# Kernel optimization log

Hardware: AMD Instinct MI355X
Metric: run time of the kernel (lower is better)

## Reference

```python
import jax, jax.numpy as jnp
import numpy as np

IN_FEATURES = 4096
OUT_FEATURES = 11008
QMIN, QMAX = -128, 127


def setup_inputs() -> dict:
    key = jax.random.key(0)
    k_in, k_w, k_s, k_z, k_b = jax.random.split(key, 5)
    inp = jax.random.normal(k_in, (4, 2048, IN_FEATURES), dtype=jnp.float32)
    # int8 quantized weight in [qmin, qmax]
    weight_quantized = jax.random.randint(
        k_w, (OUT_FEATURES, IN_FEATURES), QMIN, QMAX + 1, dtype=jnp.int32
    ).astype(jnp.int8)
    # per-output-row scale / zero point (shape [out, 1] as in the module)
    weight_scale = jax.random.uniform(k_s, (OUT_FEATURES, 1), dtype=jnp.float32,
                                      minval=0.005, maxval=0.02)
    weight_zero_point = jax.random.uniform(k_z, (OUT_FEATURES, 1), dtype=jnp.float32,
                                           minval=-4.0, maxval=4.0)
    bias = jax.random.normal(k_b, (OUT_FEATURES,), dtype=jnp.float32) * 0.01
    return {
        "input": inp,
        "weight_quantized": weight_quantized,
        "weight_scale": weight_scale,
        "weight_zero_point": weight_zero_point,
        "bias": bias,
    }


def reference(input, weight_quantized, weight_scale, weight_zero_point, bias):
    # Dequantize: per-row affine, W_f32[o, i] = (q[o, i] - zp[o]) * scale[o]
    weight_float = (weight_quantized.astype(jnp.float32) - weight_zero_point) * weight_scale
    # F.linear: y = x @ W^T + b   -> [B, S, out]
    out = jnp.einsum("bsi,oi->bso", input, weight_float) + bias
    return out
```

## Files before the change

kernel.cpp:

```cpp
#include <hip/hip_runtime.h>
#include <hip/hip_bf16.h>

#define K_DIM 4096
#define N_DIM 11008
#define M_DIM 8192

typedef _Float16 f16;
typedef f16 f16x4 __attribute__((ext_vector_type(4)));
typedef f16 f16x8 __attribute__((ext_vector_type(8)));
typedef float f32x4 __attribute__((ext_vector_type(4)));

typedef __attribute__((address_space(1))) unsigned int gu32;
typedef __attribute__((address_space(3))) unsigned int lu32;

__device__ __forceinline__ void g2l16(const void* gp, void* lp) {
    __builtin_amdgcn_global_load_lds((gu32*)gp, (lu32*)lp, 16, 0, 0);
}

__global__ __launch_bounds__(256) void convw_kernel(const int* __restrict__ Wq,
                                                    f16* __restrict__ Wh) {
    const size_t n4 = (size_t)N_DIM * K_DIM / 4;
    const size_t stride = (size_t)gridDim.x * 256;
    const int4* src = (const int4*)Wq;
    f16x4* dst = (f16x4*)Wh;
    for (size_t i = (size_t)blockIdx.x * 256 + threadIdx.x; i < n4; i += stride) {
        int4 a = src[i];
        f16x4 o = {(f16)a.x, (f16)a.y, (f16)a.z, (f16)a.w};
        dst[i] = o;
    }
}

__global__ __launch_bounds__(256) void convx_kernel(const float* __restrict__ X,
                                                    f16* __restrict__ Xh,
                                                    float* __restrict__ rs) {
    const int row = blockIdx.x;
    const int t = threadIdx.x;
    const float4* xr = (const float4*)(X + (size_t)row * K_DIM);
    f16x4* xo = (f16x4*)(Xh + (size_t)row * K_DIM);
    float s = 0.f;
#pragma unroll
    for (int j = 0; j < 4; ++j) {
        float4 v = xr[t + 256 * j];
        f16x4 h = {(f16)v.x, (f16)v.y, (f16)v.z, (f16)v.w};
        xo[t + 256 * j] = h;
        s += (float)h[0] + (float)h[1] + (float)h[2] + (float)h[3];
    }
#pragma unroll
    for (int off = 32; off > 0; off >>= 1) s += __shfl_down(s, off);
    __shared__ float part[4];
    if ((t & 63) == 0) part[t >> 6] = s;
    __syncthreads();
    if (t == 0) rs[row] = part[0] + part[1] + part[2] + part[3];
}

__global__ __launch_bounds__(256, 2)
void qlin_gemm(const f16* __restrict__ Xh, const f16* __restrict__ Wh,
               const float* __restrict__ scale, const float* __restrict__ zp,
               const float* __restrict__ bias, const float* __restrict__ rowsum,
               float* __restrict__ out) {
    __shared__ char lx[8192];
    __shared__ char lw[8192];

    const int tid = threadIdx.x;
    const int l = tid & 63;
    const int w = tid >> 6;
    const int wm = w & 1;
    const int wn = w >> 1;
    const int q = l >> 4;
    const int ln = l & 15;

    const int m0 = blockIdx.x * 128;
    const int n0 = blockIdx.y * 128;

    const int sg = (l & 3) ^ ((l >> 3) & 3);
    const size_t rowbytes = K_DIM * 2;

    const char* xg = (const char*)Xh + (size_t)(m0 + w * 16 + (l >> 2)) * rowbytes + sg * 16;
    const char* wg = (const char*)Wh + (size_t)(n0 + w * 16 + (l >> 2)) * rowbytes + sg * 16;
    char* lxp = lx + w * 1024 + l * 16;
    char* lwp = lw + w * 1024 + l * 16;

    const int rsw = (q ^ ((ln >> 1) & 3)) * 16;
    const char* lxr = lx + (wm * 64 + ln) * 64 + rsw;
    const char* lwr = lw + (wn * 64 + ln) * 64 + rsw;

    f32x4 acc[4][4] = {};

    for (int kt = 0; kt < 128; ++kt) {
        const size_t k0 = (size_t)kt * 64;
        g2l16(xg + k0, lxp);
        g2l16(xg + 64 * rowbytes + k0, lxp + 4096);
        g2l16(wg + k0, lwp);
        g2l16(wg + 64 * rowbytes + k0, lwp + 4096);
        __syncthreads();

        f16x8 af[4], bf[4];
#pragma unroll
        for (int i = 0; i < 4; ++i) af[i] = *(const f16x8*)(lxr + i * 1024);
#pragma unroll
        for (int j = 0; j < 4; ++j) bf[j] = *(const f16x8*)(lwr + j * 1024);
#pragma unroll
        for (int i = 0; i < 4; ++i)
#pragma unroll
            for (int j = 0; j < 4; ++j)
                acc[i][j] = __builtin_amdgcn_mfma_f32_16x16x32_f16(af[i], bf[j], acc[i][j], 0, 0, 0);
        __syncthreads();
    }

    float sc[4], zv[4], bv[4];
    int ncol[4];
#pragma unroll
    for (int j = 0; j < 4; ++j) {
        const int n = n0 + wn * 64 + j * 16 + ln;
        ncol[j] = n;
        sc[j] = scale[n];
        zv[j] = zp[n];
        bv[j] = bias[n];
    }
#pragma unroll
    for (int i = 0; i < 4; ++i) {
#pragma unroll
        for (int r = 0; r < 4; ++r) {
            const int m = m0 + wm * 64 + i * 16 + q * 4 + r;
            const float rsm = rowsum[m];
            const size_t rowoff = (size_t)m * N_DIM;
#pragma unroll
            for (int j = 0; j < 4; ++j) {
                out[rowoff + ncol[j]] = sc[j] * (acc[i][j][r] - zv[j] * rsm) + bv[j];
            }
        }
    }
}

extern "C" void kernel_launch(void* const* d_in, const int* in_sizes, int n_in,
                              void* d_out, int out_size, void* d_ws, size_t ws_size,
                              hipStream_t stream) {
    const float* X     = (const float*)d_in[0];
    const int*   Wq    = (const int*)d_in[1];
    const float* scale = (const float*)d_in[2];
    const float* zp    = (const float*)d_in[3];
    const float* bias  = (const float*)d_in[4];
    float* out = (float*)d_out;

    f16* Wh = (f16*)d_ws;
    f16* Xh = (f16*)((char*)d_ws + (size_t)N_DIM * K_DIM * 2);
    float* rowsum = (float*)((char*)d_ws + (size_t)N_DIM * K_DIM * 2 + (size_t)M_DIM * K_DIM * 2);

    convw_kernel<<<4096, 256, 0, stream>>>(Wq, Wh);
    convx_kernel<<<M_DIM, 256, 0, stream>>>(X, Xh, rowsum);

    dim3 grid(M_DIM / 128, N_DIM / 128);
    qlin_gemm<<<grid, 256, 0, stream>>>(Xh, Wh, scale, zp, bias, rowsum, out);
}
```

Before: 1.370 ms.

## Enlarge GEMM tile to 256x256 with double-buffered LDS and interleaved loads

```diff
diff --git a/kernel.cpp b/kernel.cpp
--- a/kernel.cpp
+++ b/kernel.cpp
@@ -1,9 +1,9 @@
 #include <hip/hip_runtime.h>
-#include <hip/hip_bf16.h>
 
 #define K_DIM 4096
 #define N_DIM 11008
 #define M_DIM 8192
+#define NT 64
 
 typedef _Float16 f16;
 typedef f16 f16x4 __attribute__((ext_vector_type(4)));
@@ -53,59 +53,128 @@
     if (t == 0) rs[row] = part[0] + part[1] + part[2] + part[3];
 }
 
-__global__ __launch_bounds__(256, 2)
+__global__ __launch_bounds__(512, 2)
 void qlin_gemm(const f16* __restrict__ Xh, const f16* __restrict__ Wh,
                const float* __restrict__ scale, const float* __restrict__ zp,
                const float* __restrict__ bias, const float* __restrict__ rowsum,
                float* __restrict__ out) {
-    __shared__ char lx[8192];
-    __shared__ char lw[8192];
-
-    const int tid = threadIdx.x;
-    const int l = tid & 63;
-    const int w = tid >> 6;
-    const int wm = w & 1;
-    const int wn = w >> 1;
+    extern __shared__ __align__(16) char smem[];
+
+    const int t = threadIdx.x;
+    const int l = t & 63;
+    const int w = t >> 6;
+    const int wm = w >> 2;
+    const int wn = w & 3;
     const int q = l >> 4;
     const int ln = l & 15;
 
-    const int m0 = blockIdx.x * 128;
-    const int n0 = blockIdx.y * 128;
-
-    const int sg = (l & 3) ^ ((l >> 3) & 3);
-    const size_t rowbytes = K_DIM * 2;
-
-    const char* xg = (const char*)Xh + (size_t)(m0 + w * 16 + (l >> 2)) * rowbytes + sg * 16;
-    const char* wg = (const char*)Wh + (size_t)(n0 + w * 16 + (l >> 2)) * rowbytes + sg * 16;
-    char* lxp = lx + w * 1024 + l * 16;
-    char* lwp = lw + w * 1024 + l * 16;
-
-    const int rsw = (q ^ ((ln >> 1) & 3)) * 16;
-    const char* lxr = lx + (wm * 64 + ln) * 64 + rsw;
-    const char* lwr = lw + (wn * 64 + ln) * 64 + rsw;
-
-    f32x4 acc[4][4] = {};
-
-    for (int kt = 0; kt < 128; ++kt) {
-        const size_t k0 = (size_t)kt * 64;
-        g2l16(xg + k0, lxp);
-        g2l16(xg + 64 * rowbytes + k0, lxp + 4096);
-        g2l16(wg + k0, lwp);
-        g2l16(wg + 64 * rowbytes + k0, lwp + 4096);
-        __syncthreads();
-
-        f16x8 af[4], bf[4];
-#pragma unroll
-        for (int i = 0; i < 4; ++i) af[i] = *(const f16x8*)(lxr + i * 1024);
-#pragma unroll
-        for (int j = 0; j < 4; ++j) bf[j] = *(const f16x8*)(lwr + j * 1024);
-#pragma unroll
-        for (int i = 0; i < 4; ++i)
-#pragma unroll
-            for (int j = 0; j < 4; ++j)
-                acc[i][j] = __builtin_amdgcn_mfma_f32_16x16x32_f16(af[i], bf[j], acc[i][j], 0, 0, 0);
-        __syncthreads();
-    }
+    const int m0 = blockIdx.x * 256;
+    const int n0 = blockIdx.y * 256;
+
+    const int srow = t >> 3;
+    const int sslot = (t & 7) ^ (srow & 7);
+    const char* xbase = (const char*)Xh + ((size_t)(m0 + srow) << 13) + (sslot << 4);
+    const char* wbase = (const char*)Wh + ((size_t)(n0 + srow) << 13) + (sslot << 4);
+    char* ldst = smem + t * 16;
+
+#define STG_A(p, c, T) g2l16(xbase + ((size_t)(c) << 19) + ((size_t)(T) << 7), ldst + (p)*65536 + (c)*8192)
+#define STG_B(p, c, T) g2l16(wbase + ((size_t)(c) << 19) + ((size_t)(T) << 7), ldst + (p)*65536 + 32768 + (c)*8192)
+#define SB __builtin_amdgcn_sched_barrier(0)
+#define BAR __builtin_amdgcn_s_barrier()
+#define LGKM0 asm volatile("s_waitcnt lgkmcnt(0)" ::: "memory")
+
+    const int xs = ln & 7;
+    int offA[2], offB[2];
+    offA[0] = (wm * 128 + ln) * 128 + ((q ^ xs) << 4);
+    offA[1] = (wm * 128 + ln) * 128 + (((q + 4) ^ xs) << 4);
+    offB[0] = 32768 + (wn * 64 + ln) * 128 + ((q ^ xs) << 4);
+    offB[1] = 32768 + (wn * 64 + ln) * 128 + (((q + 4) ^ xs) << 4);
+
+    f32x4 acc[8][4] = {};
+    f16x8 aR[4][2], bR[4][2];
+
+    STG_A(0, 0, 0); STG_A(0, 2, 0); STG_B(0, 0, 0); STG_B(0, 1, 0);
+    STG_A(0, 1, 0); STG_A(0, 3, 0); STG_B(0, 2, 0); STG_B(0, 3, 0);
+    STG_A(1, 0, 1); STG_A(1, 2, 1); STG_B(1, 0, 1); STG_B(1, 1, 1);
+    STG_A(1, 1, 1); STG_A(1, 3, 1);
+    asm volatile("s_waitcnt vmcnt(6)" ::: "memory");
+    BAR;
+
+#define TILE(T, CUR)                                                                               \
+    do {                                                                                           \
+                       \
+        _Pragma("unroll") for (int kk = 0; kk < 2; ++kk) {                                         \
+            _Pragma("unroll") for (int i = 0; i < 4; ++i)                                          \
+                aR[i][kk] = *(const f16x8*)(smem + (CUR)*65536 + offA[kk] + i * 2048);             \
+            _Pragma("unroll") for (int j = 0; j < 2; ++j)                                          \
+                bR[j][kk] = *(const f16x8*)(smem + (CUR)*65536 + offB[kk] + j * 2048);             \
+        }                                                                                          \
+        if ((T) + 1 < NT) { STG_B(((CUR) ^ 1), 2, (T) + 1); STG_B(((CUR) ^ 1), 3, (T) + 1); }      \
+        SB; BAR; LGKM0; SB;                                                                        \
+        __builtin_amdgcn_s_setprio(1);                                                             \
+        _Pragma("unroll") for (int kk = 0; kk < 2; ++kk)                                           \
+            _Pragma("unroll") for (int i = 0; i < 4; ++i)                                          \
+                _Pragma("unroll") for (int j = 0; j < 2; ++j)                                      \
+                    acc[i][j] = __builtin_amdgcn_mfma_f32_16x16x32_f16(aR[i][kk], bR[j][kk],       \
+                                                                       acc[i][j], 0, 0, 0);        \
+        __builtin_amdgcn_s_setprio(0);                                                             \
+        SB; BAR; SB;                                                                               \
+                                  \
+        _Pragma("unroll") for (int kk = 0; kk < 2; ++kk) {                                         \
+            _Pragma("unroll") for (int j = 0; j < 2; ++j)                                          \
+                bR[2 + j][kk] = *(const f16x8*)(smem + (CUR)*65536 + offB[kk] + (2 + j) * 2048);   \
+        }                                                                                          \
+        if ((T) + 2 < NT) { STG_A((CUR), 0, (T) + 2); STG_A((CUR), 2, (T) + 2); }                  \
+        SB; BAR; LGKM0; SB;                                                                        \
+        __builtin_amdgcn_s_setprio(1);                                                             \
+        _Pragma("unroll") for (int kk = 0; kk < 2; ++kk)                                           \
+            _Pragma("unroll") for (int i = 0; i < 4; ++i)                                          \
+                _Pragma("unroll") for (int j = 0; j < 2; ++j)                                      \
+                    acc[i][2 + j] = __builtin_amdgcn_mfma_f32_16x16x32_f16(aR[i][kk],              \
+                                        bR[2 + j][kk], acc[i][2 + j], 0, 0, 0);                    \
+        __builtin_amdgcn_s_setprio(0);                                                             \
+        SB; BAR; SB;                                                                               \
+                                  \
+        _Pragma("unroll") for (int kk = 0; kk < 2; ++kk) {                                         \
+            _Pragma("unroll") for (int i = 0; i < 4; ++i)                                          \
+                aR[i][kk] = *(const f16x8*)(smem + (CUR)*65536 + offA[kk] + (4 + i) * 2048);       \
+        }                                                                                          \
+        if ((T) + 2 < NT) { STG_B((CUR), 0, (T) + 2); STG_B((CUR), 1, (T) + 2); }                  \
+        SB; BAR; LGKM0; SB;                                                                        \
+        __builtin_amdgcn_s_setprio(1);                                                             \
+        _Pragma("unroll") for (int kk = 0; kk < 2; ++kk)                                           \
+            _Pragma("unroll") for (int i = 0; i < 4; ++i)                                          \
+                _Pragma("unroll") for (int j = 0; j < 2; ++j)                                      \
+                    acc[4 + i][2 + j] = __builtin_amdgcn_mfma_f32_16x16x32_f16(aR[i][kk],          \
+                                            bR[2 + j][kk], acc[4 + i][2 + j], 0, 0, 0);            \
+        __builtin_amdgcn_s_setprio(0);                                                             \
+        SB; BAR; SB;                                                                               \
+                              \
+        if ((T) + 2 < NT) {                                                                        \
+            STG_A((CUR), 1, (T) + 2); STG_A((CUR), 3, (T) + 2);                                    \
+            asm volatile("s_waitcnt vmcnt(6)" ::: "memory");                                       \
+        } else {                                                                                   \
+            asm volatile("s_waitcnt vmcnt(0)" ::: "memory");                                       \
+        }                                                                                          \
+        SB; BAR; SB;                                                                               \
+        __builtin_amdgcn_s_setprio(1);                                                             \
+        _Pragma("unroll") for (int kk = 0; kk < 2; ++kk)                                           \
+            _Pragma("unroll") for (int i = 0; i < 4; ++i)                                          \
+                _Pragma("unroll") for (int j = 0; j < 2; ++j)                                      \
+                    acc[4 + i][j] = __builtin_amdgcn_mfma_f32_16x16x32_f16(aR[i][kk], bR[j][kk],   \
+                                        acc[4 + i][j], 0, 0, 0);                                   \
+        __builtin_amdgcn_s_setprio(0);                                                             \
+        SB; BAR; SB;                                                                               \
+    } while (0)
+
+#pragma unroll 1
+    for (int Tp = 0; Tp < NT / 2; ++Tp) {
+        TILE(2 * Tp, 0);
+        TILE(2 * Tp + 1, 1);
+    }
+#undef TILE
+#undef STG_A
+#undef STG_B
 
     float sc[4], zv[4], bv[4];
     int ncol[4];
@@ -118,10 +187,10 @@
         bv[j] = bias[n];
     }
 #pragma unroll
-    for (int i = 0; i < 4; ++i) {
+    for (int i = 0; i < 8; ++i) {
 #pragma unroll
         for (int r = 0; r < 4; ++r) {
-            const int m = m0 + wm * 64 + i * 16 + q * 4 + r;
+            const int m = m0 + wm * 128 + i * 16 + q * 4 + r;
             const float rsm = rowsum[m];
             const size_t rowoff = (size_t)m * N_DIM;
 #pragma unroll
@@ -146,9 +215,16 @@
     f16* Xh = (f16*)((char*)d_ws + (size_t)N_DIM * K_DIM * 2);
     float* rowsum = (float*)((char*)d_ws + (size_t)N_DIM * K_DIM * 2 + (size_t)M_DIM * K_DIM * 2);
 
+    static bool attr_done = false;
+    if (!attr_done) {
+        (void)hipFuncSetAttribute((const void*)qlin_gemm,
+                                  hipFuncAttributeMaxDynamicSharedMemorySize, 131072);
+        attr_done = true;
+    }
+
     convw_kernel<<<4096, 256, 0, stream>>>(Wq, Wh);
     convx_kernel<<<M_DIM, 256, 0, stream>>>(X, Xh, rowsum);
 
-    dim3 grid(M_DIM / 128, N_DIM / 128);
-    qlin_gemm<<<grid, 256, 0, stream>>>(Xh, Wh, scale, zp, bias, rowsum, out);
-}
+    dim3 grid(M_DIM / 256, N_DIM / 256);
+    qlin_gemm<<<grid, 512, 131072, stream>>>(Xh, Wh, scale, zp, bias, rowsum, out);
+}
```

New measurement: 1.160 ms. 1.18x faster.
